# Kernel optimization log

Hardware: AMD Instinct MI355X
Metric: run time of the kernel (lower is better)

The kernel has to match this reference:

```python
import jax, jax.numpy as jnp
import numpy as np

C_IN = 128
D_K = 256
D_V = 256
N_HEAD = 8
H = 192
W = 192
REGION = 3
TEMPER = int(np.sqrt(D_K))  # int(sqrt(d_k)) per the torch module


def setup_inputs() -> dict:
    key = jax.random.key(0)
    k1, k2, k3, k4 = jax.random.split(key, 4)
    scale = 1.0 / np.sqrt(C_IN).astype(np.float32)
    x = jax.random.normal(k1, (1, C_IN, H, W), dtype=jnp.float32)
    wq = jax.random.normal(k2, (D_K, C_IN), dtype=jnp.float32) * scale
    wk = jax.random.normal(k3, (D_K, C_IN), dtype=jnp.float32) * scale
    wv = jax.random.normal(k4, (D_V, C_IN), dtype=jnp.float32) * scale
    return {"x": x, "wq": wq, "wk": wk, "wv": wv}


def _stretch(t):
    # Equivalent of the fixed Conv3d 'stretch' trick: for each (i, j) in the
    # 3x3 region, channel 3*i+j holds the input shifted by (i-1, j-1), zero-padded.
    # t: [b, d, H, W] -> [b, 9, d, H, W]
    b, d, h, w = t.shape
    tp = jnp.pad(t, ((0, 0), (0, 0), (1, 1), (1, 1)))
    return jnp.stack(
        [tp[:, :, i:i + h, j:j + w] for i in range(REGION) for j in range(REGION)],
        axis=1,
    )


def reference(x, wq, wk, wv):
    b = x.shape[0]  # must be 1 (module's broadcast only works for batch 1)
    dkh = D_K // N_HEAD
    dvh = D_V // N_HEAD
    r2 = REGION * REGION
    # 1x1 conv projections == channel matmuls
    q = jnp.einsum('oc,bchw->bohw', wq, x)
    k = jnp.einsum('oc,bchw->bohw', wk, x)
    v = jnp.einsum('oc,bchw->bohw', wv, x)
    Q = _stretch(q)  # [b, 9, d_k, H, W]
    K = _stretch(k)
    V = _stretch(v)  # [b, 9, d_v, H, W]
    # elementwise QK, per-head channel sum, scale, softmax over the 9 region slots
    qk = (Q * K).reshape(b, r2, N_HEAD, dkh, H, W)
    scores = jax.nn.softmax(qk.sum(axis=3) / TEMPER, axis=1)  # [b, 9, n_head, H, W]
    # dropout is identity in eval mode (att_drop disabled for the reference)
    Vh = V.reshape(b, r2, N_HEAD, dvh, H, W)
    out = (scores[:, :, :, None] * Vh).sum(axis=1).reshape(b, D_V, H, W)
    return out
```

## Files before the change

### kernel.cpp

```cpp
#include <hip/hip_runtime.h>

#define HW_   36864
#define WI    192
#define HT    192
#define CIN   128
#define DK    256
#define NH    8
#define DKH   32

using short4_ = __attribute__((ext_vector_type(4))) short;
using short8  = __attribute__((ext_vector_type(8))) short;
using float4_ = __attribute__((ext_vector_type(4))) float;

static __device__ __forceinline__ float b2f(unsigned short u) {
    union { unsigned int i; float f; } x; x.i = ((unsigned int)u) << 16; return x.f;
}
static __device__ __forceinline__ unsigned short f2b(float f) {
    union { float f; unsigned int i; } x; x.f = f;
    unsigned int r = x.i + 0x7FFFu + ((x.i >> 16) & 1u);
    return (unsigned short)(r >> 16);
}

__global__ __launch_bounds__(256) void convw_kernel(
    const float* __restrict__ wq,
    const float* __restrict__ wk,
    const float* __restrict__ wv,
    unsigned short* __restrict__ wqkv)
{
    int id = blockIdx.x * 256 + threadIdx.x;
    int h   = id / 12288;
    int rem = id - h * 12288;
    int r   = rem >> 7;
    int c   = rem & 127;
    const float* __restrict__ s = (r < 32) ? wq : ((r < 64) ? wk : wv);
    wqkv[id] = f2b(s[(h * 32 + (r & 31)) * 128 + c]);
}

__global__ __launch_bounds__(256) void projfused2_kernel(
    const float* __restrict__ x,
    const unsigned short* __restrict__ wqkv,
    unsigned short* __restrict__ vbuf,
    float* __restrict__ sbuf)
{
    __shared__ unsigned short Sh[96 * 136];
    const int px0 = blockIdx.x * 64;
    const int t   = threadIdx.x;
    const int lane = t & 63, wave = t >> 6;
    const int col  = lane & 15, quad = lane >> 4;

    #pragma unroll 4
    for (int i = 0; i < 32; ++i) {
        int id = i * 256 + t;
        int c = id >> 6, p = id & 63;
        Sh[p * 136 + c] = f2b(x[c * HW_ + px0 + p]);
    }
    __syncthreads();

    short8 bfrag[4];
    {
        int n = wave * 16 + col;
        #pragma unroll
        for (int kt = 0; kt < 4; ++kt)
            bfrag[kt] = *(const short8*)&Sh[n * 136 + kt * 32 + quad * 8];
    }

    for (int head = 0; head < 8; ++head) {
        __syncthreads();
        const unsigned short* __restrict__ Ag = wqkv + head * 96 * 128;
        #pragma unroll
        for (int i = 0; i < 6; ++i) {
            int id = i * 256 + t;
            int row = id >> 4, c8 = id & 15;
            *(short8*)&Sh[row * 136 + c8 * 8] = *(const short8*)&Ag[row * 128 + c8 * 8];
        }
        __syncthreads();

        float4_ acc[6];
        #pragma unroll
        for (int mt = 0; mt < 6; ++mt)
            acc[mt] = (float4_){0.f, 0.f, 0.f, 0.f};

        #pragma unroll
        for (int mt = 0; mt < 6; ++mt) {
            #pragma unroll
            for (int kt = 0; kt < 4; ++kt) {
                short8 a = *(const short8*)&Sh[(mt * 16 + col) * 136 + kt * 32 + quad * 8];
                acc[mt] = __builtin_amdgcn_mfma_f32_16x16x32_bf16(a, bfrag[kt], acc[mt], 0, 0, 0);
            }
        }

        int px = px0 + wave * 16 + col;
        float s = 0.f;
        #pragma unroll
        for (int reg = 0; reg < 4; ++reg)
            s += acc[0][reg] * acc[2][reg]
               + acc[1][reg] * acc[3][reg];
        s += __shfl_xor(s, 16, 64);
        s += __shfl_xor(s, 32, 64);
        if (quad == 0) sbuf[head * HW_ + px] = s;
        unsigned short* vp = vbuf + ((size_t)head * HW_ + px) * 32;
        short4_ v0, v1;
        #pragma unroll
        for (int reg = 0; reg < 4; ++reg) {
            v0[reg] = (short)f2b(acc[4][reg]);
            v1[reg] = (short)f2b(acc[5][reg]);
        }
        *(short4_*)&vp[quad * 4]      = v0;
        *(short4_*)&vp[16 + quad * 4] = v1;
    }
}

__global__ __launch_bounds__(256) void attn_kernel(
    const unsigned short* __restrict__ vbuf,
    const float* __restrict__ sbuf,
    float* __restrict__ out)
{
    __shared__ unsigned short Vh[6][18][32];
    __shared__ float Ssc[6][18];
    __shared__ float tr[32][65];

    const int b    = blockIdx.x;
    const int tile = b % 576;
    const int head = b / 576;
    const int t    = threadIdx.x;
    const int ty = tile / 12, tx = tile - ty * 12;
    const int y0 = ty * 4, x0 = tx * 16;

    const unsigned short* __restrict__ vb = vbuf + (size_t)head * HW_ * 32;
    const float* __restrict__ Sg = sbuf + head * HW_;

    for (int id = t; id < 432; id += 256) {
        int cell = id >> 2, q = id & 3;
        int hy = cell / 18, hx = cell - hy * 18;
        int gy = y0 - 1 + hy; gy = gy < 0 ? 0 : (gy > HT - 1 ? HT - 1 : gy);
        int gx = x0 - 1 + hx; gx = gx < 0 ? 0 : (gx > WI - 1 ? WI - 1 : gx);
        *(short8*)&Vh[hy][hx][q * 8] =
            *(const short8*)&vb[((size_t)(gy * WI + gx)) * 32 + q * 8];
    }
    if (t < 108) {
        int hy = t / 18, hx = t - hy * 18;
        int gy = y0 - 1 + hy; gy = gy < 0 ? 0 : (gy > HT - 1 ? HT - 1 : gy);
        int gx = x0 - 1 + hx; gx = gx < 0 ? 0 : (gx > WI - 1 ? WI - 1 : gx);
        Ssc[hy][hx] = Sg[gy * WI + gx];
    }
    __syncthreads();

    const int pxl = t >> 2;
    const int cg  = t & 3;
    const int ly  = pxl >> 4, lx = pxl & 15;
    const int y   = y0 + ly, xx = x0 + lx;

    float w[9];
    float m = -1e30f;
    #pragma unroll
    for (int r = 0; r < 9; ++r) {
        int dy = r / 3 - 1, dx = r % 3 - 1;
        int ny = y + dy, nx = xx + dx;
        bool inb = (ny >= 0) && (ny < HT) && (nx >= 0) && (nx < WI);
        float val = inb ? (Ssc[ly + dy + 1][lx + dx + 1] * 0.0625f) : 0.0f;
        w[r] = val;
        m = fmaxf(m, val);
    }
    float wsum = 0.f;
    #pragma unroll
    for (int r = 0; r < 9; ++r) {
        float e = __expf(w[r] - m);
        w[r] = e;
        wsum += e;
    }
    float inv = 1.0f / wsum;
    #pragma unroll
    for (int r = 0; r < 9; ++r) {
        int dy = r / 3 - 1, dx = r % 3 - 1;
        int ny = y + dy, nx = xx + dx;
        bool inb = (ny >= 0) && (ny < HT) && (nx >= 0) && (nx < WI);
        w[r] = inb ? (w[r] * inv) : 0.0f;
    }

    float acc[8] = {0.f, 0.f, 0.f, 0.f, 0.f, 0.f, 0.f, 0.f};
    #pragma unroll
    for (int r = 0; r < 9; ++r) {
        int dy = r / 3 - 1, dx = r % 3 - 1;
        short8 v8 = *(const short8*)&Vh[ly + dy + 1][lx + dx + 1][cg * 8];
        #pragma unroll
        for (int j = 0; j < 8; ++j)
            acc[j] = fmaf(w[r], b2f((unsigned short)v8[j]), acc[j]);
    }
    #pragma unroll
    for (int j = 0; j < 8; ++j)
        tr[cg * 8 + j][pxl] = acc[j];
    __syncthreads();

    const int ch   = t >> 3;
    const int ly2  = (t >> 1) & 3;
    const int half = t & 1;
    float4_ o0, o1;
    #pragma unroll
    for (int j = 0; j < 4; ++j) {
        o0[j] = tr[ch][ly2 * 16 + half * 8 + j];
        o1[j] = tr[ch][ly2 * 16 + half * 8 + 4 + j];
    }
    float* o = out + (size_t)(head * DKH + ch) * HW_ + (y0 + ly2) * WI + x0 + half * 8;
    *(float4_*)&o[0] = o0;
    *(float4_*)&o[4] = o1;
}

extern "C" void kernel_launch(void* const* d_in, const int* in_sizes, int n_in,
                              void* d_out, int out_size, void* d_ws, size_t ws_size,
                              hipStream_t stream) {
    const float* x  = (const float*)d_in[0];
    const float* wq = (const float*)d_in[1];
    const float* wk = (const float*)d_in[2];
    const float* wv = (const float*)d_in[3];

    char* ws = (char*)d_ws;
    unsigned short* wqkv = (unsigned short*)ws;
    unsigned short* vbuf = (unsigned short*)(ws + 196608);
    float*          sbuf = (float*)(ws + 19071104);

    convw_kernel<<<384, 256, 0, stream>>>(wq, wk, wv, wqkv);
    projfused2_kernel<<<576, 256, 0, stream>>>(x, wqkv, vbuf, sbuf);
    attn_kernel<<<4608, 256, 0, stream>>>(vbuf, sbuf, (float*)d_out);
}
```

Before: 118.0 us.

## Double-buffer per-head weight tiles and split projection waves into 2x2 M/N grid

The projection kernel now double-buffers the per-head QKV weight tile in shared memory, prefetching the next head's weights while computing the current head. That removes one barrier per head and hides the global load. Waves are rearranged into a 2x2 grid over weight rows and pixel columns, with weight rows interleaved so each wave holds matching q/k/v halves. Partial q·k sums are reduced through shared memory before sbuf is written. The cost is doubled LDS use, more B fragments held in registers, and an extra shared-memory reduction step.

```diff
diff --git a/kernel.cpp b/kernel.cpp
--- a/kernel.cpp
+++ b/kernel.cpp
@@ -32,81 +32,110 @@
     int rem = id - h * 12288;
     int r   = rem >> 7;
     int c   = rem & 127;
-    const float* __restrict__ s = (r < 32) ? wq : ((r < 64) ? wk : wv);
-    wqkv[id] = f2b(s[(h * 32 + (r & 31)) * 128 + c]);
-}
-
-__global__ __launch_bounds__(256) void projfused2_kernel(
+    int g   = r >> 4;
+    int gm  = g % 3;
+    int rr  = ((g >= 3) ? 16 : 0) + (r & 15);
+    const float* __restrict__ s = (gm == 0) ? wq : ((gm == 1) ? wk : wv);
+    wqkv[id] = f2b(s[(h * 32 + rr) * 128 + c]);
+}
+
+__global__ __launch_bounds__(256) void projfused3_kernel(
     const float* __restrict__ x,
     const unsigned short* __restrict__ wqkv,
     unsigned short* __restrict__ vbuf,
     float* __restrict__ sbuf)
 {
-    __shared__ unsigned short Sh[96 * 136];
+    __shared__ unsigned short ShA[2][96 * 136];
+    __shared__ float sP[2][2][64];
+
     const int px0 = blockIdx.x * 64;
     const int t   = threadIdx.x;
     const int lane = t & 63, wave = t >> 6;
     const int col  = lane & 15, quad = lane >> 4;
-
+    const int wm   = wave >> 1, wn = wave & 1;
+
+    unsigned short* Bs = &ShA[0][0];
     #pragma unroll 4
     for (int i = 0; i < 32; ++i) {
         int id = i * 256 + t;
         int c = id >> 6, p = id & 63;
-        Sh[p * 136 + c] = f2b(x[c * HW_ + px0 + p]);
-    }
-    __syncthreads();
-
-    short8 bfrag[4];
+        Bs[p * 136 + c] = f2b(x[c * HW_ + px0 + p]);
+    }
+    __syncthreads();
+
+    short8 bfrag[2][4];
+    #pragma unroll
+    for (int nt = 0; nt < 2; ++nt) {
+        int n = wn * 32 + nt * 16 + col;
+        #pragma unroll
+        for (int kt = 0; kt < 4; ++kt)
+            bfrag[nt][kt] = *(const short8*)&Bs[n * 136 + kt * 32 + quad * 8];
+    }
+    __syncthreads();
+
     {
-        int n = wave * 16 + col;
-        #pragma unroll
-        for (int kt = 0; kt < 4; ++kt)
-            bfrag[kt] = *(const short8*)&Sh[n * 136 + kt * 32 + quad * 8];
-    }
-
-    for (int head = 0; head < 8; ++head) {
-        __syncthreads();
-        const unsigned short* __restrict__ Ag = wqkv + head * 96 * 128;
+        const unsigned short* __restrict__ Ag = wqkv;
         #pragma unroll
         for (int i = 0; i < 6; ++i) {
             int id = i * 256 + t;
             int row = id >> 4, c8 = id & 15;
-            *(short8*)&Sh[row * 136 + c8 * 8] = *(const short8*)&Ag[row * 128 + c8 * 8];
-        }
+            *(short8*)&ShA[0][row * 136 + c8 * 8] = *(const short8*)&Ag[row * 128 + c8 * 8];
+        }
+    }
+    __syncthreads();
+
+    for (int head = 0; head < 8; ++head) {
+        if (head < 7) {
+            const unsigned short* __restrict__ Ag = wqkv + (head + 1) * 96 * 128;
+            unsigned short* __restrict__ Ad = &ShA[(head + 1) & 1][0];
+            #pragma unroll
+            for (int i = 0; i < 6; ++i) {
+                int id = i * 256 + t;
+                int row = id >> 4, c8 = id & 15;
+                *(short8*)&Ad[row * 136 + c8 * 8] = *(const short8*)&Ag[row * 128 + c8 * 8];
+            }
+        }
+        const unsigned short* __restrict__ As = &ShA[head & 1][0];
+
+        float4_ acc[3][2];
+        #pragma unroll
+        for (int mt = 0; mt < 3; ++mt) {
+            acc[mt][0] = (float4_){0.f, 0.f, 0.f, 0.f};
+            acc[mt][1] = (float4_){0.f, 0.f, 0.f, 0.f};
+        }
+
+        #pragma unroll
+        for (int mt = 0; mt < 3; ++mt) {
+            #pragma unroll
+            for (int kt = 0; kt < 4; ++kt) {
+                short8 a = *(const short8*)&As[(wm * 48 + mt * 16 + col) * 136 + kt * 32 + quad * 8];
+                acc[mt][0] = __builtin_amdgcn_mfma_f32_16x16x32_bf16(a, bfrag[0][kt], acc[mt][0], 0, 0, 0);
+                acc[mt][1] = __builtin_amdgcn_mfma_f32_16x16x32_bf16(a, bfrag[1][kt], acc[mt][1], 0, 0, 0);
+            }
+        }
+
+        #pragma unroll
+        for (int nt = 0; nt < 2; ++nt) {
+            int px = px0 + wn * 32 + nt * 16 + col;
+            float s = 0.f;
+            #pragma unroll
+            for (int reg = 0; reg < 4; ++reg)
+                s += acc[0][nt][reg] * acc[1][nt][reg];
+            s += __shfl_xor(s, 16, 64);
+            s += __shfl_xor(s, 32, 64);
+            if (quad == 0) sP[head & 1][wm][wn * 32 + nt * 16 + col] = s;
+            unsigned short* vp = vbuf + ((size_t)head * HW_ + px) * 32;
+            short4_ v0;
+            #pragma unroll
+            for (int reg = 0; reg < 4; ++reg)
+                v0[reg] = (short)f2b(acc[2][nt][reg]);
+            *(short4_*)&vp[wm * 16 + quad * 4] = v0;
+        }
+
         __syncthreads();
 
-        float4_ acc[6];
-        #pragma unroll
-        for (int mt = 0; mt < 6; ++mt)
-            acc[mt] = (float4_){0.f, 0.f, 0.f, 0.f};
-
-        #pragma unroll
-        for (int mt = 0; mt < 6; ++mt) {
-            #pragma unroll
-            for (int kt = 0; kt < 4; ++kt) {
-                short8 a = *(const short8*)&Sh[(mt * 16 + col) * 136 + kt * 32 + quad * 8];
-                acc[mt] = __builtin_amdgcn_mfma_f32_16x16x32_bf16(a, bfrag[kt], acc[mt], 0, 0, 0);
-            }
-        }
-
-        int px = px0 + wave * 16 + col;
-        float s = 0.f;
-        #pragma unroll
-        for (int reg = 0; reg < 4; ++reg)
-            s += acc[0][reg] * acc[2][reg]
-               + acc[1][reg] * acc[3][reg];
-        s += __shfl_xor(s, 16, 64);
-        s += __shfl_xor(s, 32, 64);
-        if (quad == 0) sbuf[head * HW_ + px] = s;
-        unsigned short* vp = vbuf + ((size_t)head * HW_ + px) * 32;
-        short4_ v0, v1;
-        #pragma unroll
-        for (int reg = 0; reg < 4; ++reg) {
-            v0[reg] = (short)f2b(acc[4][reg]);
-            v1[reg] = (short)f2b(acc[5][reg]);
-        }
-        *(short4_*)&vp[quad * 4]      = v0;
-        *(short4_*)&vp[16 + quad * 4] = v1;
+        if (t < 64)
+            sbuf[head * HW_ + px0 + t] = sP[head & 1][0][t] + sP[head & 1][1][t];
     }
 }
 
@@ -219,6 +248,6 @@
     float*          sbuf = (float*)(ws + 19071104);
 
     convw_kernel<<<384, 256, 0, stream>>>(wq, wk, wv, wqkv);
-    projfused2_kernel<<<576, 256, 0, stream>>>(x, wqkv, vbuf, sbuf);
+    projfused3_kernel<<<576, 256, 0, stream>>>(x, wqkv, vbuf, sbuf);
     attn_kernel<<<4608, 256, 0, stream>>>(vbuf, sbuf, (float*)d_out);
 }
```

After: 109.2 us. 1.08x faster.
